# Kernel optimization log

Measured on AMD Instinct MI355X. Metric: run time of the kernel, lower is better.

## Reference

```python
import jax, jax.numpy as jnp
import numpy as np

N_ATOM = 30000
N_PAIR = 1_000_000
N_TRI = 4_000_000
N_SF = 16
RC = 6.0

LAMBD = jnp.array([-1.0, 1.0] * 8, dtype=jnp.float32)
ZETA = jnp.array([1.0, 1.0, 2.0, 2.0, 4.0, 4.0, 8.0, 8.0] * 2, dtype=jnp.float32)
ETA = jnp.array([0.01, 0.014, 0.02, 0.028, 0.04, 0.056, 0.08, 0.11,
                 0.16, 0.22, 0.32, 0.45, 0.63, 0.72, 0.9, 1.0], dtype=jnp.float32)


def cutoff_f1(r):
    # PiNN 'f1' cutoff: 0.5*(cos(pi*r/rc)+1)
    return 0.5 * (jnp.cos(jnp.float32(np.pi) * r / RC) + 1.0)


def gaussian_basis(r, fc):
    # GaussianBasis with center=0, gamma=eta: fc * exp(-eta * r^2), shape [n, n_sf]
    return fc[:, None] * jnp.exp(-ETA[None, :] * (r[:, None] ** 2))


def setup_inputs() -> dict:
    key = jax.random.key(0)
    k1, k2, k3, k4, k5 = jax.random.split(key, 5)
    ind_2 = jax.random.randint(k1, (N_PAIR, 2), 0, N_ATOM, dtype=jnp.int32)
    ind_3 = jax.random.randint(k2, (N_TRI, 2), 0, N_PAIR, dtype=jnp.int32)
    dist = jax.random.uniform(k3, (N_PAIR,), jnp.float32, 0.5, RC)
    dirs = jax.random.normal(k4, (N_PAIR, 3), jnp.float32)
    dirs = dirs / jnp.linalg.norm(dirs, axis=1, keepdims=True)
    diff = dirs * dist[:, None]  # bond vectors consistent with dist
    elems = jax.random.randint(k5, (N_ATOM,), 0, 4, dtype=jnp.int32)
    fc = cutoff_f1(dist)
    return {"ind_2": ind_2, "ind_3": ind_3, "dist": dist, "diff": diff,
            "elems": elems, "fc": fc}


def reference(ind_2, ind_3, dist, diff, elems, fc):
    # i=j=k='ALL': species filter is identity; a_rind = arange(n_atom)
    ind_ij = ind_3[:, 0]
    ind_ik = ind_3[:, 1]
    i_rind = ind_2[ind_ij, 0]  # central atom index per triplet

    diff_ij = diff[ind_ij]  # [T,3]
    diff_ik = diff[ind_ik]
    diff_jk = diff_ik - diff_ij
    dist_jk = jnp.linalg.norm(diff_jk, axis=1)
    mask = dist_jk < RC  # TF filters triplets; we mask (jit-friendly)

    fc_jk = cutoff_f1(dist_jk)
    dist_ij = dist[ind_ij]
    dist_ik = dist[ind_ik]
    fc_ij = fc[ind_ij]
    fc_ik = fc[ind_ik]

    cos_ijk = jnp.einsum('id,id->i', diff_ij, diff_ik) / dist_ij / dist_ik
    base = jnp.maximum(1.0 + LAMBD[None, :] * cos_ijk[:, None], 0.0)
    sf = (2.0 ** (1.0 - ZETA[None, :]) * base ** ZETA[None, :]
          * gaussian_basis(dist_ij, fc_ij)
          * gaussian_basis(dist_ik, fc_ik)
          * gaussian_basis(dist_jk, fc_jk))
    sf = jnp.where(mask[:, None], sf, 0.0)

    # scatter_nd add into per-atom fingerprints
    fp = jnp.zeros((N_ATOM, N_SF), dtype=sf.dtype).at[i_rind].add(sf)

    # jacobian indices: central-atom rel index per participating pair
    vals = jnp.where(mask, i_rind, -1)
    seg = jnp.concatenate([ind_ij, ind_ik])
    pair_i = jax.ops.segment_max(jnp.concatenate([vals, vals]), seg,
                                 num_segments=N_PAIR)
    pair_i = jnp.maximum(pair_i, -1)  # empty segments -> -1 sentinel
    jacob_ind = jnp.stack([jnp.arange(N_PAIR, dtype=jnp.int32), pair_i], axis=1)
    return fp, jacob_ind
```

## Files before the change

### kernel.cpp

```cpp
#include <hip/hip_runtime.h>

#define N_ATOM 30000
#define N_PAIR 1000000
#define N_TRI  4000000
#define N_SF   16
#define FP_ELEMS (N_ATOM * N_SF)

#define ASH  5
#define APB  32
#define NCB  938
#define NSUB 8
#define NSEG (NCB * NSUB)
#define OVF_CNT_IDX NSEG
#define OVF_CAP 131072
#define TILE 4096
#define PER_TH 16
#define NTILES ((N_TRI + TILE - 1) / TILE)
#define MERGE 2
#define NRB (NCB * 4)
#define LFB 2048

#define OFF_CCNT   0ULL
#define OFF_PCNT   32768ULL
#define OFF_PPLACE 98304ULL
#define OFF_PBASE  163840ULL
#define OFF_AMAP   196608ULL
#define OFF_FLAGB  4196608ULL
#define OFF_OVF    4327680ULL
#define OFF_PACKS  5376256ULL
#define OFF_CB     21376256ULL
#define ZERO_INTS  41984
#define FLAGB_INTS 32768

__device__ __constant__ float c_eta[16] = {
    0.01f, 0.014f, 0.02f, 0.028f, 0.04f, 0.056f, 0.08f, 0.11f,
    0.16f, 0.22f, 0.32f, 0.45f, 0.63f, 0.72f, 0.9f, 1.0f};

__device__ __forceinline__ bool tri_math(
    float4 A, float4 B, float A8[8], float& R2)
{
    float ax = A.x, ay = A.y, az = A.z;
    float bx = B.x, by = B.y, bz = B.z;
    float d2ij = fmaf(ax, ax, fmaf(ay, ay, az * az));
    float d2ik = fmaf(bx, bx, fmaf(by, by, bz * bz));
    float jx = bx - ax, jy = by - ay, jz = bz - az;
    float d2jk = fmaf(jx, jx, fmaf(jy, jy, jz * jz));
    if (!(d2jk < 36.0f)) return false;
    float dij = sqrtf(d2ij);
    float dik = sqrtf(d2ik);
    float djk = sqrtf(d2jk);
    const float PI_OVER_RC = 0.5235987755982988f;
    float fcij = 0.5f * (__cosf(PI_OVER_RC * dij) + 1.0f);
    float fcik = 0.5f * (__cosf(PI_OVER_RC * dik) + 1.0f);
    float fcjk = 0.5f * (__cosf(PI_OVER_RC * djk) + 1.0f);
    float dot = fmaf(ax, bx, fmaf(ay, by, az * bz));
    float cosv = dot / (dij * dik);
    R2 = d2ij + d2ik + d2jk;
    float FCt = fcij * fcik * fcjk;
    float bm = fmaxf(1.0f - cosv, 0.0f);
    float bp = fmaxf(1.0f + cosv, 0.0f);
    float bm2 = bm * bm, bp2 = bp * bp;
    float bm4 = bm2 * bm2, bp4 = bp2 * bp2;
    float bm8 = bm4 * bm4, bp8 = bp4 * bp4;
    A8[0] = FCt * bm;               A8[1] = FCt * bp;
    A8[2] = 0.5f * FCt * bm2;       A8[3] = 0.5f * FCt * bp2;
    A8[4] = 0.125f * FCt * bm4;     A8[5] = 0.125f * FCt * bp4;
    A8[6] = 0.0078125f * FCt * bm8; A8[7] = 0.0078125f * FCt * bp8;
    return true;
}


__global__ __launch_bounds__(256) void zero_meta(
    int* __restrict__ m, unsigned int* __restrict__ fb)
{
    int i = blockIdx.x * blockDim.x + threadIdx.x;
    if (i < ZERO_INTS) m[i] = 0;
    if (i < FLAGB_INTS) fb[i] = 0u;
}

__global__ __launch_bounds__(256) void pair_hist(
    const int2* __restrict__ ind2, int* __restrict__ pcnt)
{
    __shared__ int h[NCB];
    for (int i = threadIdx.x; i < NCB; i += 256) h[i] = 0;
    __syncthreads();
    int stride = gridDim.x * 256;
    for (int p = blockIdx.x * 256 + threadIdx.x; p < N_PAIR; p += stride)
        atomicAdd(&h[ind2[p].x >> ASH], 1);
    __syncthreads();
    for (int i = threadIdx.x; i < NCB; i += 256) {
        int v = h[i];
        if (v) atomicAdd(&pcnt[i * 16], v);
    }
}

__global__ __launch_bounds__(1024) void scan_bases(
    const int* __restrict__ pcnt, int* __restrict__ pbase)
{
    __shared__ int s[1024];
    int t = threadIdx.x;
    int v0 = (t < NCB) ? pcnt[t * 16] : 0;
    s[t] = v0;
    __syncthreads();
    for (int off = 1; off < 1024; off <<= 1) {
        int v = 0;
        if (t >= off) v = s[t - off];
        __syncthreads();
        s[t] += v;
        __syncthreads();
    }
    if (t < NCB) pbase[t] = s[t] - v0;
    if (t == 0) pbase[NCB] = N_PAIR;
}

__global__ __launch_bounds__(256) void pair_place(
    const int2* __restrict__ ind2, const float* __restrict__ diff,
    const int* __restrict__ pbase, int* __restrict__ pplace,
    unsigned int* __restrict__ amap, float4* __restrict__ packs,
    float* __restrict__ out)
{
    int p = blockIdx.x * blockDim.x + threadIdx.x;
    if (p < FP_ELEMS) out[p] = 0.0f;
    if (p >= N_PAIR) return;
    int a = ind2[p].x;
    int c = a >> ASH;
    int l = atomicAdd(&pplace[c * 16], 1);
    int q = pbase[c] + l;
    amap[p] = ((unsigned)c << 22) | ((unsigned)(a & (APB - 1)) << 17) | (unsigned)l;
    float4 r;
    r.x = diff[3 * p + 0];
    r.y = diff[3 * p + 1];
    r.z = diff[3 * p + 2];
    r.w = __int_as_float(-1);
    packs[q] = r;
}

__global__ __launch_bounds__(256) void bin3(
    const int2* __restrict__ ind3, const unsigned int* __restrict__ amap,
    const int* __restrict__ pbase,
    int* __restrict__ ccnt, int2* __restrict__ cbucket,
    int2* __restrict__ ovf, int cap)
{
    __shared__ int lcnt[NCB];
    __shared__ int lbase[NCB];
    const int thr = threadIdx.x;
    const int sub = blockIdx.x & (NSUB - 1);
    const long long t0 = (long long)blockIdx.x * TILE;

    for (int i = thr; i < NCB; i += 256) lcnt[i] = 0;
    __syncthreads();

    unsigned int mij_r[PER_TH];
    int qik_r[PER_TH];
    int slot_r[PER_TH];
#pragma unroll
    for (int j = 0; j < PER_TH; ++j) {
        long long t = t0 + j * 256 + thr;
        unsigned int mij = 0; int qik = 0, s = -1;
        if (t < N_TRI) {
            int2 pr = ind3[t];
            mij = amap[pr.x];
            unsigned int mik = amap[pr.y];
            qik = pbase[mik >> 22] + (int)(mik & 0x1FFFF);
            s = atomicAdd(&lcnt[mij >> 22], 1);
        }
        mij_r[j] = mij; qik_r[j] = qik; slot_r[j] = s;
    }
    __syncthreads();
    for (int c = thr; c < NCB; c += 256) {
        int n = lcnt[c];
        lbase[c] = n ? atomicAdd(&ccnt[c * NSUB + sub], n) : 0;
    }
    __syncthreads();
#pragma unroll
    for (int j = 0; j < PER_TH; ++j) {
        long long t = t0 + j * 256 + thr;
        if (t >= N_TRI) continue;
        unsigned int mij = mij_r[j];
        int c = mij >> 22;
        int slot = lbase[c] + slot_r[j];
        if (slot < cap) {
            int2 e;
            e.x = (int)(mij & 0x3FFFFF);
            e.y = qik_r[j];
            cbucket[(size_t)(c * NSUB + sub) * cap + slot] = e;
        } else {
            int o = atomicAdd(&ccnt[OVF_CNT_IDX], 1);
            if (o < OVF_CAP) { int2 e; e.x = (int)mij; e.y = qik_r[j]; ovf[o] = e; }
        }
    }
}

__global__ __launch_bounds__(256) void reduce4(
    const int* __restrict__ ccnt, const int2* __restrict__ cbucket, int cap,
    float4* __restrict__ packs, const int* __restrict__ pbase,
    unsigned int* __restrict__ flagbits, float* __restrict__ out)
{
    __shared__ float lacc[APB * 17];
    __shared__ unsigned int lflag[LFB / 32];
    const int blk = blockIdx.x;
    const int b = blk >> 2;
    const int quad = blk & 3;
    const int thr = threadIdx.x;
    const int base = pbase[b];
    const int wlen = pbase[b + 1] - base;

    for (int i = thr; i < APB * 17; i += 256) lacc[i] = 0.0f;
    if (thr < LFB / 32) lflag[thr] = 0u;

    const int seg0 = b * NSUB + quad * MERGE;
    const int n0 = min(ccnt[seg0 + 0], cap);
    const int n1 = min(ccnt[seg0 + 1], cap);
    const int m = n0 + n1;
    const int2* segp0 = cbucket + (size_t)seg0 * cap;
    int* pw = (int*)packs;
    __syncthreads();

    for (int j0 = 0; j0 < m; j0 += 512) {
        int i1 = j0 + thr;
        int i2 = i1 + 256;
        bool v1 = i1 < m, v2 = i2 < m;
        int jc1 = v1 ? i1 : m - 1;
        int jc2 = v2 ? i2 : m - 1;
        int s1 = jc1 >= n0, s2 = jc2 >= n0;
        int2 e1 = segp0[(size_t)s1 * cap + (jc1 - (s1 ? n0 : 0))];
        int2 e2 = segp0[(size_t)s2 * cap + (jc2 - (s2 ? n0 : 0))];
        int l1 = e1.x & 0x1FFFF;
        int l2 = e2.x & 0x1FFFF;
        float4 B1 = packs[e1.y];
        float4 B2 = packs[e2.y];
        float4 A1 = packs[base + l1];
        float4 A2 = packs[base + l2];

        float A8[8], R2v;
        if (v1 && tri_math(A1, B1, A8, R2v)) {
            int a5 = (e1.x >> 17) & (APB - 1);
            if (l1 < LFB) atomicOr(&lflag[l1 >> 5], 1u << (l1 & 31));
            else { int g = base + l1; atomicOr(&flagbits[g >> 5], 1u << (g & 31)); }
            atomicMax(&pw[4 * e1.y + 3], (b << ASH) + a5);
#pragma unroll
            for (int s = 0; s < 16; ++s)
                atomicAdd(&lacc[a5 * 17 + s], A8[s & 7] * __expf(-c_eta[s] * R2v));
        }
        if (v2 && tri_math(A2, B2, A8, R2v)) {
            int a5 = (e2.x >> 17) & (APB - 1);
            if (l2 < LFB) atomicOr(&lflag[l2 >> 5], 1u << (l2 & 31));
            else { int g = base + l2; atomicOr(&flagbits[g >> 5], 1u << (g & 31)); }
            atomicMax(&pw[4 * e2.y + 3], (b << ASH) + a5);
#pragma unroll
            for (int s = 0; s < 16; ++s)
                atomicAdd(&lacc[a5 * 17 + s], A8[s & 7] * __expf(-c_eta[s] * R2v));
        }
    }
    __syncthreads();

    {
        int sh = base & 31;
        int w0 = base >> 5;
        int nw = (min(wlen, LFB) + 31) >> 5;
        for (int i = thr; i < nw; i += 256) {
            unsigned int w = lflag[i];
            if (!w) continue;
            atomicOr(&flagbits[w0 + i], w << sh);
            if (sh) {
                unsigned int hi = w >> (32 - sh);
                if (hi) atomicOr(&flagbits[w0 + i + 1], hi);
            }
        }
    }
    for (int t = thr; t < APB * N_SF; t += 256) {
        int atom = (b << ASH) + (t >> 4);
        float v = lacc[(t >> 4) * 17 + (t & 15)];
        if (atom < N_ATOM && v != 0.0f)
            unsafeAtomicAdd(out + (size_t)atom * N_SF + (t & 15), v);
    }
}

__global__ __launch_bounds__(256) void ovf3(
    const int* __restrict__ ccnt, const int2* __restrict__ ovf,
    float4* __restrict__ packs, const int* __restrict__ pbase,
    unsigned int* __restrict__ flagbits, float* __restrict__ out)
{
    int i = blockIdx.x * blockDim.x + threadIdx.x;
    int n = ccnt[OVF_CNT_IDX];
    if (n > OVF_CAP) n = OVF_CAP;
    if (i >= n) return;
    int2 e = ovf[i];
    unsigned int mij = (unsigned int)e.x;
    int qik = e.y;
    int c = mij >> 22;
    int a5 = (mij >> 17) & (APB - 1);
    int lidx = mij & 0x1FFFF;
    int qij = pbase[c] + lidx;
    float4 A = packs[qij];
    float4 B = packs[qik];
    float A8[8], R2;
    if (!tri_math(A, B, A8, R2)) return;
    int atom = (c << ASH) + a5;
    int* pw = (int*)packs;
    atomicOr(&flagbits[qij >> 5], 1u << (qij & 31));
    atomicMax(&pw[4 * qik + 3], atom);
    float* basep = out + (size_t)atom * N_SF;
#pragma unroll
    for (int s = 0; s < 16; ++s)
        unsafeAtomicAdd(basep + s, A8[s & 7] * __expf(-c_eta[s] * R2));
}

__global__ __launch_bounds__(256) void fin3(
    const unsigned int* __restrict__ amap, const int* __restrict__ pbase,
    const float4* __restrict__ packs, const unsigned int* __restrict__ flagbits,
    float* __restrict__ out)
{
    int p = blockIdx.x * blockDim.x + threadIdx.x;
    if (p >= N_PAIR) return;
    unsigned int mm = amap[p];
    int c = mm >> 22;
    int lidx = (int)(mm & 0x1FFFF);
    int a5 = (mm >> 17) & (APB - 1);
    int q = pbase[c] + lidx;
    int w = ((const int*)packs)[4 * q + 3];
    unsigned int fb = flagbits[q >> 5];
    int a = (c << ASH) + a5;
    int v = ((fb >> (q & 31)) & 1u) ? max(w, a) : w;
    float* jf = out + FP_ELEMS;
    jf[2 * p + 0] = (float)p;
    jf[2 * p + 1] = (float)v;
}


__global__ __launch_bounds__(256) void init_legacy(float* __restrict__ out) {
    int i = blockIdx.x * blockDim.x + threadIdx.x;
    if (i < FP_ELEMS) out[i] = 0.0f;
    if (i < N_PAIR) ((int*)out + FP_ELEMS)[2 * i + 1] = -1;
}

__global__ __launch_bounds__(256) void tri_legacy(
    const int* __restrict__ ind2, const int2* __restrict__ ind3,
    const float* __restrict__ dist, const float* __restrict__ diff,
    const float* __restrict__ fc, float* __restrict__ out) {
    int t = blockIdx.x * blockDim.x + threadIdx.x;
    if (t >= N_TRI) return;
    int2 pr = ind3[t];
    int ij = pr.x, ik = pr.y;
    float4 A, B;
    A.x = diff[3 * ij + 0]; A.y = diff[3 * ij + 1]; A.z = diff[3 * ij + 2]; A.w = 0.f;
    B.x = diff[3 * ik + 0]; B.y = diff[3 * ik + 1]; B.z = diff[3 * ik + 2]; B.w = 0.f;
    float A8[8], R2;
    if (!tri_math(A, B, A8, R2)) return;
    int atom = ind2[2 * ij];
    int* jac = (int*)out + FP_ELEMS;
    atomicMax(&jac[2 * ij + 1], atom);
    atomicMax(&jac[2 * ik + 1], atom);
    float* base = out + (size_t)atom * N_SF;
#pragma unroll
    for (int s = 0; s < 16; ++s)
        unsafeAtomicAdd(base + s, A8[s & 7] * __expf(-c_eta[s] * R2));
}

__global__ __launch_bounds__(256) void fin_legacy(float* __restrict__ out) {
    int p = blockIdx.x * blockDim.x + threadIdx.x;
    if (p >= N_PAIR) return;
    int* jac = (int*)out + FP_ELEMS;
    int v = jac[2 * p + 1];
    float* jf = (float*)jac;
    jf[2 * p + 0] = (float)p;
    jf[2 * p + 1] = (float)v;
}


extern "C" void kernel_launch(void* const* d_in, const int* in_sizes, int n_in,
                              void* d_out, int out_size, void* d_ws, size_t ws_size,
                              hipStream_t stream) {
    const int2*  ind2 = (const int2*)d_in[0];
    const int2*  ind3 = (const int2*)d_in[1];
    const float* dist = (const float*)d_in[2];
    const float* diff = (const float*)d_in[3];
    const float* fc   = (const float*)d_in[5];
    float* out = (float*)d_out;

    const size_t seg_stride = (size_t)NSEG * sizeof(int2);
    const size_t need_min = OFF_CB + seg_stride * 608;

    if (ws_size >= need_min) {
        char* ws = (char*)d_ws;
        int* ccnt            = (int*)(ws + OFF_CCNT);
        int* pcnt            = (int*)(ws + OFF_PCNT);
        int* pplace          = (int*)(ws + OFF_PPLACE);
        int* pbase           = (int*)(ws + OFF_PBASE);
        unsigned int* amap   = (unsigned int*)(ws + OFF_AMAP);
        unsigned int* flagb  = (unsigned int*)(ws + OFF_FLAGB);
        int2* ovf            = (int2*)(ws + OFF_OVF);
        float4* packs        = (float4*)(ws + OFF_PACKS);
        int2* cbucket        = (int2*)(ws + OFF_CB);
        int cap = (int)((ws_size - OFF_CB) / seg_stride);
        if (cap > 1024) cap = 1024;

        int pb = (N_PAIR + 255) / 256;
        zero_meta<<<(ZERO_INTS + 255) / 256, 256, 0, stream>>>((int*)ws, flagb);
        pair_hist<<<240, 256, 0, stream>>>(ind2, pcnt);
        scan_bases<<<1, 1024, 0, stream>>>(pcnt, pbase);
        pair_place<<<pb, 256, 0, stream>>>(ind2, diff, pbase, pplace, amap, packs, out);
        bin3<<<NTILES, 256, 0, stream>>>(ind3, amap, pbase, ccnt, cbucket, ovf, cap);
        reduce4<<<NRB, 256, 0, stream>>>(ccnt, cbucket, cap, packs, pbase, flagb, out);
        ovf3<<<OVF_CAP / 256, 256, 0, stream>>>(ccnt, ovf, packs, pbase, flagb, out);
        fin3<<<pb, 256, 0, stream>>>(amap, pbase, packs, flagb, out);
    } else {
        init_legacy<<<(N_PAIR + 255) / 256, 256, 0, stream>>>(out);
        tri_legacy<<<(N_TRI + 255) / 256, 256, 0, stream>>>((const int*)d_in[0], ind3, dist, diff, fc, out);
        fin_legacy<<<(N_PAIR + 255) / 256, 256, 0, stream>>>(out);
    }
    (void)dist; (void)fc; (void)in_sizes; (void)n_in; (void)out_size;
}
```

Baseline: 526.6 us.

## Shard triplet buckets by ik-pair range and stage ij pairs in shared memory

Result: slower. 565.0 us (+7.3%).

```diff
diff --git a/kernel.cpp b/kernel.cpp
--- a/kernel.cpp
+++ b/kernel.cpp
@@ -16,8 +16,7 @@
 #define TILE 4096
 #define PER_TH 16
 #define NTILES ((N_TRI + TILE - 1) / TILE)
-#define MERGE 2
-#define NRB (NCB * 4)
+#define WCAP 1280
 #define LFB 2048
 
 #define OFF_CCNT   0ULL
@@ -69,6 +68,10 @@
     return true;
 }
 
+__device__ __forceinline__ int qshard(int qik) {
+    return (int)((unsigned)(qik * 8u) / 1000000u);
+}
+
 
 __global__ __launch_bounds__(256) void zero_meta(
     int* __restrict__ m, unsigned int* __restrict__ fb)
@@ -141,13 +144,11 @@
     int* __restrict__ ccnt, int2* __restrict__ cbucket,
     int2* __restrict__ ovf, int cap)
 {
-    __shared__ int lcnt[NCB];
-    __shared__ int lbase[NCB];
+    __shared__ int lseg[NSEG];
     const int thr = threadIdx.x;
-    const int sub = blockIdx.x & (NSUB - 1);
     const long long t0 = (long long)blockIdx.x * TILE;
 
-    for (int i = thr; i < NCB; i += 256) lcnt[i] = 0;
+    for (int i = thr; i < NSEG; i += 256) lseg[i] = 0;
     __syncthreads();
 
     unsigned int mij_r[PER_TH];
@@ -162,14 +163,14 @@
             mij = amap[pr.x];
             unsigned int mik = amap[pr.y];
             qik = pbase[mik >> 22] + (int)(mik & 0x1FFFF);
-            s = atomicAdd(&lcnt[mij >> 22], 1);
+            s = atomicAdd(&lseg[(int)(mij >> 22) * NSUB + qshard(qik)], 1);
         }
         mij_r[j] = mij; qik_r[j] = qik; slot_r[j] = s;
     }
     __syncthreads();
-    for (int c = thr; c < NCB; c += 256) {
-        int n = lcnt[c];
-        lbase[c] = n ? atomicAdd(&ccnt[c * NSUB + sub], n) : 0;
+    for (int i = thr; i < NSEG; i += 256) {
+        int n = lseg[i];
+        lseg[i] = n ? atomicAdd(&ccnt[i], n) : 0;
     }
     __syncthreads();
 #pragma unroll
@@ -177,16 +178,17 @@
         long long t = t0 + j * 256 + thr;
         if (t >= N_TRI) continue;
         unsigned int mij = mij_r[j];
-        int c = mij >> 22;
-        int slot = lbase[c] + slot_r[j];
+        int qik = qik_r[j];
+        int idx = (int)(mij >> 22) * NSUB + qshard(qik);
+        int slot = lseg[idx] + slot_r[j];
         if (slot < cap) {
             int2 e;
             e.x = (int)(mij & 0x3FFFFF);
-            e.y = qik_r[j];
-            cbucket[(size_t)(c * NSUB + sub) * cap + slot] = e;
+            e.y = qik;
+            cbucket[(size_t)idx * cap + slot] = e;
         } else {
             int o = atomicAdd(&ccnt[OVF_CNT_IDX], 1);
-            if (o < OVF_CAP) { int2 e; e.x = (int)mij; e.y = qik_r[j]; ovf[o] = e; }
+            if (o < OVF_CAP) { int2 e; e.x = (int)mij; e.y = qik; ovf[o] = e; }
         }
     }
 }
@@ -196,48 +198,45 @@
     float4* __restrict__ packs, const int* __restrict__ pbase,
     unsigned int* __restrict__ flagbits, float* __restrict__ out)
 {
+    __shared__ float4 win[WCAP];
     __shared__ float lacc[APB * 17];
     __shared__ unsigned int lflag[LFB / 32];
-    const int blk = blockIdx.x;
-    const int b = blk >> 2;
-    const int quad = blk & 3;
+    const int seg = blockIdx.x;
+    const int b = seg >> 3;
     const int thr = threadIdx.x;
     const int base = pbase[b];
-    const int wlen = pbase[b + 1] - base;
+    const int wlen = min(pbase[b + 1] - base, WCAP);
 
     for (int i = thr; i < APB * 17; i += 256) lacc[i] = 0.0f;
     if (thr < LFB / 32) lflag[thr] = 0u;
-
-    const int seg0 = b * NSUB + quad * MERGE;
-    const int n0 = min(ccnt[seg0 + 0], cap);
-    const int n1 = min(ccnt[seg0 + 1], cap);
-    const int m = n0 + n1;
-    const int2* segp0 = cbucket + (size_t)seg0 * cap;
+    for (int i = thr; i < wlen; i += 256) win[i] = packs[base + i];
+
+    int n = min(ccnt[seg], cap);
+    const int2* segp = cbucket + (size_t)seg * cap;
     int* pw = (int*)packs;
     __syncthreads();
 
-    for (int j0 = 0; j0 < m; j0 += 512) {
+    for (int j0 = 0; j0 < n; j0 += 512) {
         int i1 = j0 + thr;
         int i2 = i1 + 256;
-        bool v1 = i1 < m, v2 = i2 < m;
-        int jc1 = v1 ? i1 : m - 1;
-        int jc2 = v2 ? i2 : m - 1;
-        int s1 = jc1 >= n0, s2 = jc2 >= n0;
-        int2 e1 = segp0[(size_t)s1 * cap + (jc1 - (s1 ? n0 : 0))];
-        int2 e2 = segp0[(size_t)s2 * cap + (jc2 - (s2 ? n0 : 0))];
+        bool v1 = i1 < n, v2 = i2 < n;
+        int2 e1 = segp[v1 ? i1 : n - 1];
+        int2 e2 = segp[v2 ? i2 : n - 1];
         int l1 = e1.x & 0x1FFFF;
         int l2 = e2.x & 0x1FFFF;
         float4 B1 = packs[e1.y];
         float4 B2 = packs[e2.y];
-        float4 A1 = packs[base + l1];
-        float4 A2 = packs[base + l2];
+        float4 A1 = (l1 < WCAP) ? win[l1] : packs[base + l1];
+        float4 A2 = (l2 < WCAP) ? win[l2] : packs[base + l2];
 
         float A8[8], R2v;
         if (v1 && tri_math(A1, B1, A8, R2v)) {
             int a5 = (e1.x >> 17) & (APB - 1);
             if (l1 < LFB) atomicOr(&lflag[l1 >> 5], 1u << (l1 & 31));
             else { int g = base + l1; atomicOr(&flagbits[g >> 5], 1u << (g & 31)); }
-            atomicMax(&pw[4 * e1.y + 3], (b << ASH) + a5);
+            int cand = (b << ASH) + a5;
+            if (cand > __float_as_int(B1.w))
+                atomicMax(&pw[4 * e1.y + 3], cand);
 #pragma unroll
             for (int s = 0; s < 16; ++s)
                 atomicAdd(&lacc[a5 * 17 + s], A8[s & 7] * __expf(-c_eta[s] * R2v));
@@ -246,7 +245,9 @@
             int a5 = (e2.x >> 17) & (APB - 1);
             if (l2 < LFB) atomicOr(&lflag[l2 >> 5], 1u << (l2 & 31));
             else { int g = base + l2; atomicOr(&flagbits[g >> 5], 1u << (g & 31)); }
-            atomicMax(&pw[4 * e2.y + 3], (b << ASH) + a5);
+            int cand = (b << ASH) + a5;
+            if (cand > __float_as_int(B2.w))
+                atomicMax(&pw[4 * e2.y + 3], cand);
 #pragma unroll
             for (int s = 0; s < 16; ++s)
                 atomicAdd(&lacc[a5 * 17 + s], A8[s & 7] * __expf(-c_eta[s] * R2v));
@@ -257,7 +258,7 @@
     {
         int sh = base & 31;
         int w0 = base >> 5;
-        int nw = (min(wlen, LFB) + 31) >> 5;
+        int nw = (min(pbase[b + 1] - base, LFB) + 31) >> 5;
         for (int i = thr; i < nw; i += 256) {
             unsigned int w = lflag[i];
             if (!w) continue;
@@ -401,7 +402,7 @@
         scan_bases<<<1, 1024, 0, stream>>>(pcnt, pbase);
         pair_place<<<pb, 256, 0, stream>>>(ind2, diff, pbase, pplace, amap, packs, out);
         bin3<<<NTILES, 256, 0, stream>>>(ind3, amap, pbase, ccnt, cbucket, ovf, cap);
-        reduce4<<<NRB, 256, 0, stream>>>(ccnt, cbucket, cap, packs, pbase, flagb, out);
+        reduce4<<<NSEG, 256, 0, stream>>>(ccnt, cbucket, cap, packs, pbase, flagb, out);
         ovf3<<<OVF_CAP / 256, 256, 0, stream>>>(ccnt, ovf, packs, pbase, flagb, out);
         fin3<<<pb, 256, 0, stream>>>(amap, pbase, packs, flagb, out);
     } else {
```
